# Kernel tuning notes

Hardware: AMD Instinct MI355X
Metric: run time of the kernel (lower is better)

Reference implementation:

```python
import jax, jax.numpy as jnp
import numpy as np

HIDDEN = 4096
NQ = 32        # query heads
NKV = 8        # kv heads
HD = 128       # head dim
EPS = 1e-6
BASE = 10000.0
T = 2048


def setup_inputs() -> dict:
    key = jax.random.key(0)
    ks = jax.random.split(key, 4)
    s = 0.02
    return {
        "hidden_states": jax.random.normal(ks[0], (T, HIDDEN), jnp.float32),
        "w_qkv": jax.random.normal(ks[1], ((NQ + 2 * NKV) * HD, HIDDEN), jnp.float32) * s,
        "q_norm_w": jnp.ones((HD,), jnp.float32),
        "k_norm_w": jnp.ones((HD,), jnp.float32),
        "w_o": jax.random.normal(ks[2], (HIDDEN, NQ * HD), jnp.float32) * s,
        "positions": jnp.arange(T, dtype=jnp.int64),
    }


def _rms_norm(x, w):
    # x: [T, H, D], normalize over last dim
    var = jnp.mean(jnp.square(x), axis=-1, keepdims=True)
    return x * jax.lax.rsqrt(var + EPS) * w


def _rope(x, positions):
    # neox-style: split halves. x: [T, H, D]
    half = HD // 2
    inv_freq = 1.0 / (BASE ** (jnp.arange(0, HD, 2, dtype=jnp.float32) / HD))  # [half]
    ang = positions.astype(jnp.float32)[:, None] * inv_freq  # [T, half]
    cos = jnp.cos(ang)[:, None, :]  # [T, 1, half]
    sin = jnp.sin(ang)[:, None, :]
    x1, x2 = x[..., :half], x[..., half:]
    return jnp.concatenate([x1 * cos - x2 * sin, x2 * cos + x1 * sin], axis=-1)


def reference(hidden_states, w_qkv, q_norm_w, k_norm_w, w_o, positions):
    t = hidden_states.shape[0]
    qkv = hidden_states @ w_qkv.T  # [T, (NQ+2*NKV)*HD]
    q, k, v = jnp.split(qkv, [NQ * HD, (NQ + NKV) * HD], axis=-1)
    q = _rms_norm(q.reshape(t, NQ, HD), q_norm_w)
    k = _rms_norm(k.reshape(t, NKV, HD), k_norm_w)
    v = v.reshape(t, NKV, HD)
    q = _rope(q, positions)
    k = _rope(k, positions)

    g = NQ // NKV
    qg = q.reshape(t, NKV, g, HD).transpose(1, 2, 0, 3)  # [NKV, g, T, HD]
    kt = k.transpose(1, 0, 2)  # [NKV, T, HD]
    vt = v.transpose(1, 0, 2)
    scale = HD ** -0.5
    scores = jnp.einsum('hgqd,hkd->hgqk', qg, kt) * scale  # [NKV, g, T, T]
    causal = positions[:, None] >= positions[None, :]  # [T, T]
    scores = jnp.where(causal[None, None], scores, jnp.float32(-1e30))
    p = jax.nn.softmax(scores, axis=-1)
    o = jnp.einsum('hgqk,hkd->hgqd', p, vt)  # [NKV, g, T, HD]
    o = o.transpose(2, 0, 1, 3).reshape(t, NQ * HD)
    return o @ w_o.T
```

## Files before the change

kernel.cpp:

```cpp
#include <hip/hip_runtime.h>
#include <hip/hip_bf16.h>

typedef float f32x4 __attribute__((ext_vector_type(4)));
typedef short s16x8 __attribute__((ext_vector_type(8)));
typedef short s16x4 __attribute__((ext_vector_type(4)));
typedef unsigned short u16;

#define HIDDEN 4096
#define NQ 32
#define NKV 8
#define HD 128
#define T_SEQ 2048
#define QKV_N ((NQ + 2 * NKV) * HD)

__device__ __forceinline__ u16 f2bf(float f) {
    union { float f; unsigned u; } v; v.f = f;
    unsigned r = v.u + 0x7FFFu + ((v.u >> 16) & 1u);
    return (u16)(r >> 16);
}
__device__ __forceinline__ float b2f(u16 h) {
    union { unsigned u; float f; } v; v.u = ((unsigned)h) << 16; return v.f;
}
__device__ __forceinline__ void gload_lds16(const u16* g, u16* l) {
    __builtin_amdgcn_global_load_lds(
        (const __attribute__((address_space(1))) unsigned int*)g,
        (__attribute__((address_space(3))) unsigned int*)l,
        16, 0, 0);
}
__device__ __forceinline__ int xcd_swz(int flat, int nwg) {
    return (flat & 7) * (nwg >> 3) + (flat >> 3);
}

__device__ __forceinline__ void conv8(const float* src, u16* dst, int i) {
    const float4 a = ((const float4*)src)[2 * i];
    const float4 b = ((const float4*)src)[2 * i + 1];
    s16x8 o;
    o[0] = (short)f2bf(a.x); o[1] = (short)f2bf(a.y);
    o[2] = (short)f2bf(a.z); o[3] = (short)f2bf(a.w);
    o[4] = (short)f2bf(b.x); o[5] = (short)f2bf(b.y);
    o[6] = (short)f2bf(b.z); o[7] = (short)f2bf(b.w);
    ((s16x8*)dst)[i] = o;
}
__global__ __launch_bounds__(256) void conv2_bf16_kern(
    const float* __restrict__ s1, u16* __restrict__ d1, int n1,
    const float* __restrict__ s2, u16* __restrict__ d2, int n2)
{
    for (int i = blockIdx.x * 256 + threadIdx.x; i < n1 + n2; i += gridDim.x * 256) {
        if (i < n1) conv8(s1, d1, i);
        else        conv8(s2, d2, i - n1);
    }
}

template<int NI, int OUT_BF16>
__global__ __launch_bounds__(512) void gemm_8ph(
    const u16* __restrict__ A, const u16* __restrict__ B,
    void* __restrict__ Cv, int N, int K)
{
    __shared__ u16 As[2][256 * 64];
    __shared__ u16 Bs[2][NI * 64 * 64];
    const int tid = threadIdx.x, lane = tid & 63, wid = tid >> 6;
    const int wr = wid >> 2, wc = wid & 3;
    const int lg = lane >> 4, l15 = lane & 15;
    const int m0 = blockIdx.y * 256, n0 = blockIdx.x * (NI * 64);
    const int nk = K >> 6;
    const int r8 = lane >> 3;
    const int csw = ((lane & 7) ^ r8) * 8;

    f32x4 acc[8][NI] = {};
    s16x8 af[4], bq0[NI], bq1[NI];

    auto stageA = [&](int sl, int c, int kt) {
        gload_lds16(&A[(size_t)(m0 + c * 64 + wid * 8 + r8) * K + kt * 64 + csw],
                    &As[sl][(c * 64 + wid * 8) * 64]);
    };
    auto stageB = [&](int sl, int c, int kt) {
        gload_lds16(&B[(size_t)(n0 + c * 64 + wid * 8 + r8) * K + kt * 64 + csw],
                    &Bs[sl][(c * 64 + wid * 8) * 64]);
    };
    auto ldA = [&](int s_, int mh_, int kh_) {
#pragma unroll
        for (int mi = 0; mi < 4; ++mi)
            af[mi] = *(const s16x8*)&As[s_][
                ((wr * 128 + mh_ * 64 + mi * 16 + l15) << 6) +
                (((lg + kh_ * 4) ^ (l15 & 7)) << 3)];
    };
    auto ldB = [&](int s_, int kh_, s16x8 (&bq)[NI]) {
#pragma unroll
        for (int ni = 0; ni < NI; ++ni)
            bq[ni] = *(const s16x8*)&Bs[s_][
                ((wc * (NI * 16) + ni * 16 + l15) << 6) +
                (((lg + kh_ * 4) ^ (l15 & 7)) << 3)];
    };
    auto mm = [&](int mh_, s16x8 (&bq)[NI]) {
        __builtin_amdgcn_s_setprio(1);
#pragma unroll
        for (int mi = 0; mi < 4; ++mi)
#pragma unroll
            for (int ni = 0; ni < NI; ++ni)
                acc[mh_ * 4 + mi][ni] =
                    __builtin_amdgcn_mfma_f32_16x16x32_bf16(
                        af[mi], bq[ni], acc[mh_ * 4 + mi][ni], 0, 0, 0);
        __builtin_amdgcn_s_setprio(0);
    };
#define MIDSYNC                                               \
    asm volatile("" ::: "memory");                            \
    __builtin_amdgcn_s_barrier();                             \
    asm volatile("s_waitcnt lgkmcnt(0)" ::: "memory");        \
    __builtin_amdgcn_sched_barrier(0);

    stageA(0, 0, 0); stageA(0, 1, 0); stageA(0, 2, 0); stageA(0, 3, 0);
#pragma unroll
    for (int c = 0; c < NI; ++c) stageB(0, c, 0);
    stageA(1, 0, 1); stageA(1, 2, 1);
    asm volatile("s_waitcnt vmcnt(2)" ::: "memory");
    __builtin_amdgcn_s_barrier();

    for (int t = 0; t < nk; ++t) {
        const int s = t & 1;
        ldA(s, 0, 0); ldB(s, 0, bq0);
        if (t + 1 < nk) { stageA(s ^ 1, 1, t + 1); stageA(s ^ 1, 3, t + 1); }
        MIDSYNC
        mm(0, bq0);
        __builtin_amdgcn_s_barrier();
        ldA(s, 0, 1); ldB(s, 1, bq1);
        if (t + 1 < nk) {
#pragma unroll
            for (int c = 0; c < NI; ++c) stageB(s ^ 1, c, t + 1);
        }
        MIDSYNC
        mm(0, bq1);
        __builtin_amdgcn_s_barrier();
        ldA(s, 1, 0);
        if (t + 2 < nk) { stageA(s, 0, t + 2); stageA(s, 2, t + 2); }
        MIDSYNC
        mm(1, bq0);
        __builtin_amdgcn_s_barrier();
        ldA(s, 1, 1);
        MIDSYNC
        mm(1, bq1);
        if (t + 2 < nk) asm volatile("s_waitcnt vmcnt(2)" ::: "memory");
        else            asm volatile("s_waitcnt vmcnt(0)" ::: "memory");
        asm volatile("" ::: "memory");
        __builtin_amdgcn_s_barrier();
    }
#undef MIDSYNC

#pragma unroll
    for (int mh = 0; mh < 2; ++mh)
#pragma unroll
    for (int mi = 0; mi < 4; ++mi)
#pragma unroll
    for (int ni = 0; ni < NI; ++ni) {
        int row0 = m0 + wr * 128 + mh * 64 + mi * 16 + lg * 4;
        int col  = n0 + wc * (NI * 16) + ni * 16 + l15;
#pragma unroll
        for (int r = 0; r < 4; ++r) {
            if (OUT_BF16)
                ((u16*)Cv)[(size_t)(row0 + r) * N + col] = f2bf(acc[mh * 4 + mi][ni][r]);
            else
                ((float*)Cv)[(size_t)(row0 + r) * N + col] = acc[mh * 4 + mi][ni][r];
        }
    }
}

__global__ __launch_bounds__(256) void nr_vt_kern(
    const u16* __restrict__ qkv, const float* __restrict__ qw,
    const float* __restrict__ kw, u16* __restrict__ qr, u16* __restrict__ kr,
    u16* __restrict__ vt)
{
    __shared__ u16 Ts[128][66];
    const int id = blockIdx.x, tid = threadIdx.x;
    if (id < 20480) {
        const int t = id & 2047, h = (id >> 11) * 4 + (tid >> 6);
        const int i = tid & 63;
        const size_t rowbase = (size_t)t * QKV_N;
        const u16* src; const float* w; u16* dst;
        if (h < 32) {
            src = qkv + rowbase + h * HD; w = qw;
            dst = qr + ((size_t)h * T_SEQ + t) * HD;
        } else {
            int kh = h - 32;
            src = qkv + rowbase + NQ * HD + kh * HD; w = kw;
            dst = kr + ((size_t)kh * T_SEQ + t) * HD;
        }
        float x1 = b2f(src[i]), x2 = b2f(src[i + 64]);
        float ss = x1 * x1 + x2 * x2;
#pragma unroll
        for (int d = 32; d >= 1; d >>= 1) ss += __shfl_xor(ss, d);
        float rs = rsqrtf(ss * (1.0f / 128.0f) + 1e-6f);
        x1 *= rs * w[i];
        x2 *= rs * w[i + 64];
        float ang = (float)t * exp2f((float)i * -0.20762050593567985f);
        float sn, cs;
        sincosf(ang, &sn, &cs);
        dst[i]      = f2bf(x1 * cs - x2 * sn);
        dst[i + 64] = f2bf(x2 * cs + x1 * sn);
        return;
    }
    const int id2 = id - 20480;
    const int t0 = (id2 & 31) * 64, kh = id2 >> 5;
#pragma unroll
    for (int it = 0; it < 4; ++it) {
        int slot = tid + it * 256;
        int tl = slot >> 4, dc = (slot & 15) * 8;
        s16x8 v = *(const s16x8*)&qkv[(size_t)(t0 + tl) * QKV_N + (NQ + NKV) * HD + kh * HD + dc];
#pragma unroll
        for (int e = 0; e < 8; ++e) Ts[dc + e][tl] = (u16)v[e];
    }
    __syncthreads();
#pragma unroll
    for (int it = 0; it < 4; ++it) {
        int slot = tid + it * 256;
        int d = slot >> 3, c = (slot & 7) * 8;
        s16x8 v = *(const s16x8*)&Ts[d][c];
        *(s16x8*)&vt[((size_t)kh * HD + d) * T_SEQ + t0 + c] = v;
    }
}

#define KS(b, r, c) Ks[(b)][((r) << 7) + ((c) ^ (((r) & 7) << 3))]
#define VS(b, r, c) Vs[(b)][((r) << 6) + ((c) ^ (((r) & 7) << 3))]
#define PS(wv, r, c) Ps[((wv) << 10) + ((r) << 6) + ((c) ^ (((r) & 7) << 3))]

__global__ __launch_bounds__(512) void attn_kern(
    const u16* __restrict__ qr, const u16* __restrict__ kr,
    const u16* __restrict__ vt, u16* __restrict__ o,
    const float* __restrict__ wo, u16* __restrict__ wo_bf)
{
    __shared__ u16 Ks[2][64 * 128];
    __shared__ u16 Vs[2][128 * 64];
    __shared__ u16 Ps[8 * 16 * 64];
    const int tid = threadIdx.x, lane = tid & 63, w = tid >> 6;
    const int lg = lane >> 4, l15 = lane & 15;
    const int fb = (int)blockIdx.y * 8 + (int)blockIdx.x;
    const int flat = xcd_swz(fb, 256);
    const int qh = flat >> 3, bx = flat & 7;
    const int kvh = qh >> 2;
    const float scale2 = 0.08838834764831845f * 1.4426950408889634f;

    const int cvbase = fb * 8192 + tid;
    int cv = 0;
    float4 cva = {}, cvb = {};

    const int krow = tid >> 4, kcol = (tid & 15) * 8;
    const int vrow = tid >> 3, vcol = (tid & 7) * 8;
    const u16* krbase = kr + (size_t)kvh * T_SEQ * HD;
    const u16* vtbase = vt + (size_t)kvh * HD * T_SEQ;

    s16x8 kst[2], vst[2];
#define LOADKV(k0_) do { \
    kst[0] = *(const s16x8*)&krbase[(size_t)((k0_) + krow) * HD + kcol]; \
    kst[1] = *(const s16x8*)&krbase[(size_t)((k0_) + krow + 32) * HD + kcol]; \
    vst[0] = *(const s16x8*)&vtbase[(size_t)(vrow) * T_SEQ + (k0_) + vcol]; \
    vst[1] = *(const s16x8*)&vtbase[(size_t)(vrow + 64) * T_SEQ + (k0_) + vcol]; \
    } while (0)
#define WRITEKV(b) do { \
    *(s16x8*)&KS((b), krow, kcol) = kst[0]; \
    *(s16x8*)&KS((b), krow + 32, kcol) = kst[1]; \
    *(s16x8*)&VS((b), vrow, vcol) = vst[0]; \
    *(s16x8*)&VS((b), vrow + 64, vcol) = vst[1]; \
    } while (0)

    for (int half = 0; half < 2; ++half) {
        const int q0 = (half == 0) ? bx * 128 : (T_SEQ - 128) - bx * 128;
        s16x8 qf[4];
        {
            const u16* qb = qr + ((size_t)qh * T_SEQ + q0 + w * 16 + l15) * HD;
#pragma unroll
            for (int dc = 0; dc < 4; ++dc) qf[dc] = *(const s16x8*)&qb[dc * 32 + lg * 8];
        }
        f32x4 oacc[8] = {};
        float mQ = -1e30f, lsQ = 0.f;

        const int ktiles = (q0 >> 6) + 2;
        LOADKV(0);
        WRITEKV(0);
        __syncthreads();
        for (int kt = 0; kt < ktiles; ++kt) {
            const int k0 = kt * 64;
            const int cur = kt & 1;
            if (kt + 1 < ktiles) LOADKV(k0 + 64);

            if (cv <= 16) {
                if (cv > 0) {
                    s16x8 o8;
                    o8[0] = (short)f2bf(cva.x); o8[1] = (short)f2bf(cva.y);
                    o8[2] = (short)f2bf(cva.z); o8[3] = (short)f2bf(cva.w);
                    o8[4] = (short)f2bf(cvb.x); o8[5] = (short)f2bf(cvb.y);
                    o8[6] = (short)f2bf(cvb.z); o8[7] = (short)f2bf(cvb.w);
                    ((s16x8*)wo_bf)[cvbase + (cv - 1) * 512] = o8;
                }
                if (cv < 16) {
                    cva = ((const float4*)wo)[2 * (cvbase + cv * 512)];
                    cvb = ((const float4*)wo)[2 * (cvbase + cv * 512) + 1];
                }
                ++cv;
            }

            f32x4 sc[4] = {};
            __builtin_amdgcn_s_setprio(1);
#pragma unroll
            for (int nc = 0; nc < 4; ++nc)
#pragma unroll
                for (int dc = 0; dc < 4; ++dc) {
                    s16x8 kf = *(const s16x8*)&KS(cur, nc * 16 + l15, dc * 32 + lg * 8);
                    sc[nc] = __builtin_amdgcn_mfma_f32_16x16x32_bf16(kf, qf[dc], sc[nc], 0, 0, 0);
                }
            __builtin_amdgcn_s_setprio(0);

            const int qg = q0 + w * 16 + l15;
            const bool needMask = (k0 + 63) > (q0 + w * 16);
            float tm = -1e30f;
#pragma unroll
            for (int nc = 0; nc < 4; ++nc)
#pragma unroll
                for (int r = 0; r < 4; ++r) {
                    float v = sc[nc][r] * scale2;
                    int kg = k0 + nc * 16 + lg * 4 + r;
                    if (needMask && kg > qg) v = -1e30f;
                    sc[nc][r] = v;
                    tm = fmaxf(tm, v);
                }
            tm = fmaxf(tm, __shfl_xor(tm, 16));
            tm = fmaxf(tm, __shfl_xor(tm, 32));

            if (__any(tm > mQ + 8.0f)) {
                float mn = fmaxf(mQ, tm);
                float alpha = exp2f(mQ - mn);
                mQ = mn;
                lsQ *= alpha;
                float aq[4];
#pragma unroll
                for (int r = 0; r < 4; ++r) aq[r] = __shfl(alpha, lg * 4 + r);
#pragma unroll
                for (int dc = 0; dc < 8; ++dc)
#pragma unroll
                    for (int r = 0; r < 4; ++r) oacc[dc][r] *= aq[r];
            }

            float ts = 0.f;
#pragma unroll
            for (int nc = 0; nc < 4; ++nc) {
                s16x4 pk;
#pragma unroll
                for (int r = 0; r < 4; ++r) {
                    float e = exp2f(sc[nc][r] - mQ);
                    ts += e;
                    pk[r] = (short)f2bf(e);
                }
                *(s16x4*)&PS(w, l15, nc * 16 + lg * 4) = pk;
            }
            ts += __shfl_xor(ts, 16);
            ts += __shfl_xor(ts, 32);
            lsQ += ts;

            __builtin_amdgcn_s_setprio(1);
#pragma unroll
            for (int kc = 0; kc < 2; ++kc) {
                s16x8 pf = *(const s16x8*)&PS(w, l15, kc * 32 + lg * 8);
#pragma unroll
                for (int dc = 0; dc < 8; ++dc) {
                    s16x8 vf = *(const s16x8*)&VS(cur, dc * 16 + l15, kc * 32 + lg * 8);
                    oacc[dc] = __builtin_amdgcn_mfma_f32_16x16x32_bf16(pf, vf, oacc[dc], 0, 0, 0);
                }
            }
            __builtin_amdgcn_s_setprio(0);

            if (kt + 1 < ktiles) WRITEKV(cur ^ 1);
            __syncthreads();
        }
        float lq[4];
#pragma unroll
        for (int r = 0; r < 4; ++r) lq[r] = __shfl(lsQ, lg * 4 + r);
#pragma unroll
        for (int r = 0; r < 4; ++r) {
            float inv = 1.0f / lq[r];
            int trow = q0 + w * 16 + lg * 4 + r;
            u16* dst = o + (size_t)trow * (NQ * HD) + qh * HD;
#pragma unroll
            for (int dc = 0; dc < 8; ++dc) dst[dc * 16 + l15] = f2bf(oacc[dc][r] * inv);
        }
    }
#undef LOADKV
#undef WRITEKV
}

extern "C" void kernel_launch(void* const* d_in, const int* in_sizes, int n_in,
                              void* d_out, int out_size, void* d_ws, size_t ws_size,
                              hipStream_t stream)
{
    const float* hs   = (const float*)d_in[0];
    const float* wqkv = (const float*)d_in[1];
    const float* qw   = (const float*)d_in[2];
    const float* kw   = (const float*)d_in[3];
    const float* wo   = (const float*)d_in[4];
    float* out = (float*)d_out;

    char* ws = (char*)d_ws;
    u16* hs_bf   = (u16*)(ws);
    u16* ob      = (u16*)(ws);
    u16* qkv_bf  = (u16*)(ws + 16777216);
    u16* wo_bf   = (u16*)(ws + 16777216);
    u16* wqkv_bf = (u16*)(ws + 41943040);
    u16* qr      = (u16*)(ws + 67108864);
    u16* kr      = (u16*)(ws + 83886080);
    u16* vt      = (u16*)(ws + 88080384);

    conv2_bf16_kern<<<2048, 256, 0, stream>>>(
        hs, hs_bf, T_SEQ * HIDDEN / 8, wqkv, wqkv_bf, QKV_N * HIDDEN / 8);
    gemm_8ph<3, 1><<<dim3(QKV_N / 192, T_SEQ / 256), 512, 0, stream>>>(
        hs_bf, wqkv_bf, (void*)qkv_bf, QKV_N, HIDDEN);
    nr_vt_kern<<<20736, 256, 0, stream>>>(qkv_bf, qw, kw, qr, kr, vt);
    attn_kern<<<dim3(8, NQ), 512, 0, stream>>>(qr, kr, vt, ob, wo, wo_bf);
    gemm_8ph<2, 0><<<dim3(HIDDEN / 128, T_SEQ / 256), 512, 0, stream>>>(
        ob, wo_bf, (void*)out, HIDDEN, HIDDEN);
}
```

Baseline: 329.0 us.

## Restructure GEMM main loop from eight to four phases with larger fragment loads

```diff
diff --git a/kernel.cpp b/kernel.cpp
--- a/kernel.cpp
+++ b/kernel.cpp
@@ -52,7 +52,7 @@
 }
 
 template<int NI, int OUT_BF16>
-__global__ __launch_bounds__(512) void gemm_8ph(
+__global__ __launch_bounds__(512) void gemm_4ph(
     const u16* __restrict__ A, const u16* __restrict__ B,
     void* __restrict__ Cv, int N, int K)
 {
@@ -67,7 +67,7 @@
     const int csw = ((lane & 7) ^ r8) * 8;
 
     f32x4 acc[8][NI] = {};
-    s16x8 af[4], bq0[NI], bq1[NI];
+    s16x8 af[4][2], bq[NI][2];
 
     auto stageA = [&](int sl, int c, int kt) {
         gload_lds16(&A[(size_t)(m0 + c * 64 + wid * 8 + r8) * K + kt * 64 + csw],
@@ -77,36 +77,38 @@
         gload_lds16(&B[(size_t)(n0 + c * 64 + wid * 8 + r8) * K + kt * 64 + csw],
                     &Bs[sl][(c * 64 + wid * 8) * 64]);
     };
-    auto ldA = [&](int s_, int mh_, int kh_) {
+    auto ldA2 = [&](int s_, int mh_) {
 #pragma unroll
         for (int mi = 0; mi < 4; ++mi)
-            af[mi] = *(const s16x8*)&As[s_][
-                ((wr * 128 + mh_ * 64 + mi * 16 + l15) << 6) +
-                (((lg + kh_ * 4) ^ (l15 & 7)) << 3)];
+#pragma unroll
+            for (int kh = 0; kh < 2; ++kh)
+                af[mi][kh] = *(const s16x8*)&As[s_][
+                    ((wr * 128 + mh_ * 64 + mi * 16 + l15) << 6) +
+                    (((lg + kh * 4) ^ (l15 & 7)) << 3)];
     };
-    auto ldB = [&](int s_, int kh_, s16x8 (&bq)[NI]) {
+    auto ldB2 = [&](int s_) {
 #pragma unroll
         for (int ni = 0; ni < NI; ++ni)
-            bq[ni] = *(const s16x8*)&Bs[s_][
-                ((wc * (NI * 16) + ni * 16 + l15) << 6) +
-                (((lg + kh_ * 4) ^ (l15 & 7)) << 3)];
+#pragma unroll
+            for (int kh = 0; kh < 2; ++kh)
+                bq[ni][kh] = *(const s16x8*)&Bs[s_][
+                    ((wc * (NI * 16) + ni * 16 + l15) << 6) +
+                    (((lg + kh * 4) ^ (l15 & 7)) << 3)];
     };
-    auto mm = [&](int mh_, s16x8 (&bq)[NI]) {
+    auto mm2 = [&](int mh_) {
         __builtin_amdgcn_s_setprio(1);
 #pragma unroll
         for (int mi = 0; mi < 4; ++mi)
 #pragma unroll
             for (int ni = 0; ni < NI; ++ni)
-                acc[mh_ * 4 + mi][ni] =
-                    __builtin_amdgcn_mfma_f32_16x16x32_bf16(
-                        af[mi], bq[ni], acc[mh_ * 4 + mi][ni], 0, 0, 0);
+#pragma unroll
+                for (int kh = 0; kh < 2; ++kh)
+                    acc[mh_ * 4 + mi][ni] =
+                        __builtin_amdgcn_mfma_f32_16x16x32_bf16(
+                            af[mi][kh], bq[ni][kh], acc[mh_ * 4 + mi][ni], 0, 0, 0);
         __builtin_amdgcn_s_setprio(0);
     };
-#define MIDSYNC                                               \
-    asm volatile("" ::: "memory");                            \
-    __builtin_amdgcn_s_barrier();                             \
-    asm volatile("s_waitcnt lgkmcnt(0)" ::: "memory");        \
-    __builtin_amdgcn_sched_barrier(0);
+#define FENCE asm volatile("" ::: "memory");
 
     stageA(0, 0, 0); stageA(0, 1, 0); stageA(0, 2, 0); stageA(0, 3, 0);
 #pragma unroll
@@ -117,33 +119,28 @@
 
     for (int t = 0; t < nk; ++t) {
         const int s = t & 1;
-        ldA(s, 0, 0); ldB(s, 0, bq0);
-        if (t + 1 < nk) { stageA(s ^ 1, 1, t + 1); stageA(s ^ 1, 3, t + 1); }
-        MIDSYNC
-        mm(0, bq0);
+        ldA2(s, 0); ldB2(s);
+        if (t + 1 < nk) {
+            stageA(s ^ 1, 1, t + 1); stageA(s ^ 1, 3, t + 1);
+#pragma unroll
+            for (int c = 0; c < NI; ++c) stageB(s ^ 1, c, t + 1);
+        }
+        FENCE
         __builtin_amdgcn_s_barrier();
-        ldA(s, 0, 1); ldB(s, 1, bq1);
-        if (t + 1 < nk) {
-#pragma unroll
-            for (int c = 0; c < NI; ++c) stageB(s ^ 1, c, t + 1);
-        }
-        MIDSYNC
-        mm(0, bq1);
+        mm2(0);
+        FENCE
         __builtin_amdgcn_s_barrier();
-        ldA(s, 1, 0);
+        ldA2(s, 1);
         if (t + 2 < nk) { stageA(s, 0, t + 2); stageA(s, 2, t + 2); }
-        MIDSYNC
-        mm(1, bq0);
+        FENCE
         __builtin_amdgcn_s_barrier();
-        ldA(s, 1, 1);
-        MIDSYNC
-        mm(1, bq1);
+        mm2(1);
         if (t + 2 < nk) asm volatile("s_waitcnt vmcnt(2)" ::: "memory");
         else            asm volatile("s_waitcnt vmcnt(0)" ::: "memory");
-        asm volatile("" ::: "memory");
+        FENCE
         __builtin_amdgcn_s_barrier();
     }
-#undef MIDSYNC
+#undef FENCE
 
 #pragma unroll
     for (int mh = 0; mh < 2; ++mh)
@@ -407,10 +404,10 @@
 
     conv2_bf16_kern<<<2048, 256, 0, stream>>>(
         hs, hs_bf, T_SEQ * HIDDEN / 8, wqkv, wqkv_bf, QKV_N * HIDDEN / 8);
-    gemm_8ph<3, 1><<<dim3(QKV_N / 192, T_SEQ / 256), 512, 0, stream>>>(
+    gemm_4ph<3, 1><<<dim3(QKV_N / 192, T_SEQ / 256), 512, 0, stream>>>(
         hs_bf, wqkv_bf, (void*)qkv_bf, QKV_N, HIDDEN);
     nr_vt_kern<<<20736, 256, 0, stream>>>(qkv_bf, qw, kw, qr, kr, vt);
     attn_kern<<<dim3(8, NQ), 512, 0, stream>>>(qr, kr, vt, ob, wo, wo_bf);
-    gemm_8ph<2, 0><<<dim3(HIDDEN / 128, T_SEQ / 256), 512, 0, stream>>>(
+    gemm_4ph<2, 0><<<dim3(HIDDEN / 128, T_SEQ / 256), 512, 0, stream>>>(
         ob, wo_bf, (void*)out, HIDDEN, HIDDEN);
 }
```

Result: faster. 303.6 us (-7.7%).
